# Kernel optimization log

Hardware: AMD Instinct MI355X
Metric: run time of the kernel (lower is better)

## Reference

```python
import jax, jax.numpy as jnp
import numpy as np

SEQ_LEN = 4096
PRED_LEN = 4096
D_MODEL = 512
PERIOD = 32
N = SEQ_LEN // PERIOD   # 128
M = PRED_LEN // PERIOD  # 128
K = 2 * (PERIOD // 2) + 1  # 33
B = 32


def setup_inputs() -> dict:
    key = jax.random.key(0)
    k1, k2, k3 = jax.random.split(key, 3)
    h = jax.random.normal(k1, (B, SEQ_LEN, D_MODEL), dtype=jnp.float32)
    # torch Conv1d weight layout: [out_ch, in_ch/groups, k] = [D, 1, K]
    conv_w = jax.random.normal(k2, (D_MODEL, 1, K), dtype=jnp.float32) * (1.0 / np.sqrt(K))
    # torch Linear(n, m, bias=False) weight: [m, n]
    backbone_w = jax.random.normal(k3, (M, N), dtype=jnp.float32) * (1.0 / np.sqrt(N))
    return {"h": h, "conv_w": conv_w, "backbone_w": backbone_w}


def reference(h, conv_w, backbone_w):
    Bb, L, D = h.shape
    w, n, m, H = PERIOD, N, M, PRED_LEN
    h_t = jnp.transpose(h, (0, 2, 1))  # [B, D, L]
    conv = jax.lax.conv_general_dilated(
        h_t, conv_w,
        window_strides=(1,),
        padding=[(K // 2, K // 2)],
        dimension_numbers=("NCH", "OIH", "NCH"),
        feature_group_count=D,
    )
    h_agg = h_t + conv  # residual depthwise conv, [B, D, L]
    # rearrange into phases: [B*D, n, w] -> [B*D, w, n]
    x_by_phase = jnp.transpose(h_agg.reshape(Bb * D, n, w), (0, 2, 1))
    # per-phase linear n -> m (Linear weight is [m, n], applied as x @ W^T)
    y_by_phase = jnp.einsum("pwn,mn->pwm", x_by_phase, backbone_w)  # [B*D, w, m]
    # de-interleave phases back into a length-H sequence
    y_reordered = jnp.transpose(y_by_phase, (0, 2, 1)).reshape(Bb * D, H)
    y = jnp.transpose(y_reordered.reshape(Bb, D, H), (0, 2, 1))  # [B, H, D]
    return y
```

## Files before the change

### kernel.cpp

```cpp
#include <hip/hip_runtime.h>

#define SEQ_LEN 4096
#define D_MODEL 512
#define KSZ 33

typedef __attribute__((ext_vector_type(4))) float float4v;
typedef __attribute__((ext_vector_type(8))) short short8;

static __device__ __forceinline__ unsigned short f2bf(float f) {
    unsigned int u = __float_as_uint(f);
    u += 0x7fffu + ((u >> 16) & 1u);
    return (unsigned short)(u >> 16);
}

__global__ __launch_bounds__(256) void k_prep(const float* __restrict__ bw,
                                              unsigned short* __restrict__ wb) {
    int i = blockIdx.x * 256 + threadIdx.x;
    if (i < 128 * 128) wb[i] = f2bf(bw[i]);
}

__global__ __launch_bounds__(256) void k_conv(const float* __restrict__ h,
                                              const float* __restrict__ cw,
                                              float* __restrict__ hagg) {
    __shared__ float tile[96][64];
    __shared__ float wsh[64][33];

    const int lt = blockIdx.x, dt = blockIdx.y, b = blockIdx.z;
    const int tid = threadIdx.x;
    const int c = tid & 63;
    const int l0 = lt * 64;

    const float* hb = h + ((size_t)b * SEQ_LEN) * D_MODEL + dt * 64;
    for (int r = (tid >> 6); r < 96; r += 4) {
        int l = l0 - 16 + r;
        float v = 0.f;
        if (l >= 0 && l < SEQ_LEN) v = hb[(size_t)l * D_MODEL + c];
        tile[r][c] = v;
    }
    for (int idx = tid; idx < 64 * KSZ; idx += 256) {
        int dd = idx / KSZ, k = idx - dd * KSZ;
        wsh[dd][k] = cw[(size_t)(dt * 64 + dd) * KSZ + k];
    }
    __syncthreads();

    const int lsub = (tid >> 6) * 16;

    float buf[16];
#pragma unroll
    for (int j = 0; j < 16; j++) buf[j] = tile[lsub + j][c];

    float acc[16] = {};
#pragma unroll
    for (int k = 0; k < KSZ; k++) {
        float wk = wsh[c][k] + ((k == 16) ? 1.0f : 0.0f);
#pragma unroll
        for (int j = 0; j < 16; j++) acc[j] += wk * buf[(k + j) & 15];
        if (k < 32) buf[k & 15] = tile[lsub + k + 16][c];
    }

    float* ob = hagg + ((size_t)b * SEQ_LEN + l0 + lsub) * D_MODEL + dt * 64 + c;
#pragma unroll
    for (int j = 0; j < 16; j++) ob[(size_t)j * D_MODEL] = acc[j];
}

#define XSTR 136
__global__ __launch_bounds__(256, 2) void k_gemm(const unsigned short* __restrict__ wb,
                                                 float* __restrict__ outp) {
    __shared__ unsigned short xl[256 * XSTR];

    const int tid = threadIdx.x;
    const int dh = blockIdx.x, ph = blockIdx.y, b = blockIdx.z;
    const int lane = tid & 63, w = tid >> 6;

    {
        const float* xrow0 = outp + ((size_t)(b * SEQ_LEN) + ph) * D_MODEL
                           + dh * 256 + lane * 4;
#pragma unroll
        for (int p = 0; p < 16; p++) {
            int ip = p * 4 + w;
            int i0 = ip * 2;
            const float* src = xrow0 + (size_t)i0 * 32 * D_MODEL;
            float4v v0 = *(const float4v*)(src);
            float4v v1 = *(const float4v*)(src + 32 * D_MODEL);
            int ib = i0 >> 3;
            int wof = i0 & 7;
#pragma unroll
            for (int dd = 0; dd < 4; dd++) {
                int d = lane * 4 + dd;
                unsigned int pk = (unsigned int)f2bf(v0[dd])
                                | ((unsigned int)f2bf(v1[dd]) << 16);
                int off = d * XSTR + (((ib ^ (d >> 3)) & 15) << 3) + wof;
                *(unsigned int*)(&xl[off]) = pk;
            }
        }
    }
    __syncthreads();

    const int q = lane >> 4, r16 = lane & 15;

    float4v acc[2][16] = {};
#pragma unroll
    for (int kb = 0; kb < 128; kb += 32) {
        short8 a[2];
#pragma unroll
        for (int mt = 0; mt < 2; mt++) {
            int row = w * 32 + mt * 16 + r16;
            a[mt] = *(const short8*)(wb + row * 128 + kb + q * 8);
        }
#pragma unroll
        for (int dtl = 0; dtl < 16; dtl++) {
            int d = dtl * 16 + r16;
            int ib = (kb >> 3) + q;
            short8 bfrag = *(const short8*)(&xl[d * XSTR + (((ib ^ (d >> 3)) & 15) << 3)]);
#pragma unroll
            for (int mt = 0; mt < 2; mt++)
                acc[mt][dtl] = __builtin_amdgcn_mfma_f32_16x16x32_bf16(
                    a[mt], bfrag, acc[mt][dtl], 0, 0, 0);
        }
    }

    float* ob = outp + ((size_t)b * SEQ_LEN) * D_MODEL;
#pragma unroll
    for (int mt = 0; mt < 2; mt++) {
        int mbase = w * 32 + mt * 16 + q * 4;
#pragma unroll
        for (int r = 0; r < 4; r++) {
            int m = mbase + r;
            int hidx = m * 32 + ph;
#pragma unroll
            for (int dtl = 0; dtl < 16; dtl++) {
                int d = dh * 256 + dtl * 16 + r16;
                ob[(size_t)hidx * D_MODEL + d] = acc[mt][dtl][r];
            }
        }
    }
}

extern "C" void kernel_launch(void* const* d_in, const int* in_sizes, int n_in,
                              void* d_out, int out_size, void* d_ws, size_t ws_size,
                              hipStream_t stream) {
    const float* h  = (const float*)d_in[0];
    const float* cw = (const float*)d_in[1];
    const float* bw = (const float*)d_in[2];
    float* out = (float*)d_out;

    unsigned short* wb = (unsigned short*)d_ws;

    k_prep<<<dim3(64), 256, 0, stream>>>(bw, wb);
    k_conv<<<dim3(64, 8, 32), 256, 0, stream>>>(h, cw, out);
    k_gemm<<<dim3(2, 32, 32), 256, 0, stream>>>(wb, out);
}
```

Baseline: 740.9 us.

## Transpose conv weights in prep, widen GEMM blocks, and stage output stores through LDS

The prep kernel now writes a transposed copy of the conv weights, so the conv kernel reads per-channel weights directly with coalesced global loads instead of staging them in shared memory. Empty asm barriers keep the input buffer values pinned in registers. The GEMM kernel moves to 512 threads with one 16-row M tile per wave, batches its global loads before the bf16 conversion, and writes its output through an LDS transpose so each wave issues float4 row stores instead of scattered scalar stores. This adds extra barriers and LDS traffic in exchange for better-coalesced output writes and higher occupancy.

Measured after the change: 693.7 us. 6.4% less time.

```diff
diff --git a/kernel.cpp b/kernel.cpp
--- a/kernel.cpp
+++ b/kernel.cpp
@@ -14,16 +14,21 @@
 }
 
 __global__ __launch_bounds__(256) void k_prep(const float* __restrict__ bw,
-                                              unsigned short* __restrict__ wb) {
+                                              const float* __restrict__ cw,
+                                              unsigned short* __restrict__ wb,
+                                              float* __restrict__ wt) {
     int i = blockIdx.x * 256 + threadIdx.x;
     if (i < 128 * 128) wb[i] = f2bf(bw[i]);
+    if (i < KSZ * D_MODEL) {
+        int k = i >> 9, d = i & 511;
+        wt[i] = cw[(size_t)d * KSZ + k];
+    }
 }
 
 __global__ __launch_bounds__(256) void k_conv(const float* __restrict__ h,
-                                              const float* __restrict__ cw,
+                                              const float* __restrict__ wt,
                                               float* __restrict__ hagg) {
     __shared__ float tile[96][64];
-    __shared__ float wsh[64][33];
 
     const int lt = blockIdx.x, dt = blockIdx.y, b = blockIdx.z;
     const int tid = threadIdx.x;
@@ -37,25 +42,28 @@
         if (l >= 0 && l < SEQ_LEN) v = hb[(size_t)l * D_MODEL + c];
         tile[r][c] = v;
     }
-    for (int idx = tid; idx < 64 * KSZ; idx += 256) {
-        int dd = idx / KSZ, k = idx - dd * KSZ;
-        wsh[dd][k] = cw[(size_t)(dt * 64 + dd) * KSZ + k];
-    }
     __syncthreads();
 
     const int lsub = (tid >> 6) * 16;
+    const float* wcol = wt + dt * 64 + c;
 
     float buf[16];
 #pragma unroll
-    for (int j = 0; j < 16; j++) buf[j] = tile[lsub + j][c];
+    for (int j = 0; j < 16; j++) {
+        buf[j] = tile[lsub + j][c];
+        asm volatile("" : "+v"(buf[j]));
+    }
 
     float acc[16] = {};
 #pragma unroll
     for (int k = 0; k < KSZ; k++) {
-        float wk = wsh[c][k] + ((k == 16) ? 1.0f : 0.0f);
+        float wk = wcol[(size_t)k * D_MODEL] + ((k == 16) ? 1.0f : 0.0f);
 #pragma unroll
         for (int j = 0; j < 16; j++) acc[j] += wk * buf[(k + j) & 15];
-        if (k < 32) buf[k & 15] = tile[lsub + k + 16][c];
+        if (k < 32) {
+            buf[k & 15] = tile[lsub + k + 16][c];
+            asm volatile("" : "+v"(buf[k & 15]));
+        }
     }
 
     float* ob = hagg + ((size_t)b * SEQ_LEN + l0 + lsub) * D_MODEL + dt * 64 + c;
@@ -64,9 +72,9 @@
 }
 
 #define XSTR 136
-__global__ __launch_bounds__(256, 2) void k_gemm(const unsigned short* __restrict__ wb,
+__global__ __launch_bounds__(512, 4) void k_gemm(const unsigned short* __restrict__ wb,
                                                  float* __restrict__ outp) {
-    __shared__ unsigned short xl[256 * XSTR];
+    __shared__ __attribute__((aligned(16))) unsigned short xl[256 * XSTR];
 
     const int tid = threadIdx.x;
     const int dh = blockIdx.x, ph = blockIdx.y, b = blockIdx.z;
@@ -76,21 +84,27 @@
         const float* xrow0 = outp + ((size_t)(b * SEQ_LEN) + ph) * D_MODEL
                            + dh * 256 + lane * 4;
 #pragma unroll
-        for (int p = 0; p < 16; p++) {
-            int ip = p * 4 + w;
-            int i0 = ip * 2;
-            const float* src = xrow0 + (size_t)i0 * 32 * D_MODEL;
-            float4v v0 = *(const float4v*)(src);
-            float4v v1 = *(const float4v*)(src + 32 * D_MODEL);
-            int ib = i0 >> 3;
-            int wof = i0 & 7;
+        for (int c2 = 0; c2 < 2; c2++) {
+            float4v va[4], vb[4];
 #pragma unroll
-            for (int dd = 0; dd < 4; dd++) {
-                int d = lane * 4 + dd;
-                unsigned int pk = (unsigned int)f2bf(v0[dd])
-                                | ((unsigned int)f2bf(v1[dd]) << 16);
-                int off = d * XSTR + (((ib ^ (d >> 3)) & 15) << 3) + wof;
-                *(unsigned int*)(&xl[off]) = pk;
+            for (int pp = 0; pp < 4; pp++) {
+                int ip = (c2 * 4 + pp) * 8 + w;
+                const float* src = xrow0 + (size_t)(ip * 2) * 32 * D_MODEL;
+                va[pp] = *(const float4v*)(src);
+                vb[pp] = *(const float4v*)(src + 32 * D_MODEL);
+            }
+#pragma unroll
+            for (int pp = 0; pp < 4; pp++) {
+                int i0 = ((c2 * 4 + pp) * 8 + w) * 2;
+                int ib = i0 >> 3, wof = i0 & 7;
+#pragma unroll
+                for (int dd = 0; dd < 4; dd++) {
+                    int d = lane * 4 + dd;
+                    unsigned int pk = (unsigned int)f2bf(va[pp][dd])
+                                    | ((unsigned int)f2bf(vb[pp][dd]) << 16);
+                    int off = d * XSTR + (((ib ^ (d >> 3)) & 15) << 3) + wof;
+                    *(unsigned int*)(&xl[off]) = pk;
+                }
             }
         }
     }
@@ -98,41 +112,41 @@
 
     const int q = lane >> 4, r16 = lane & 15;
 
-    float4v acc[2][16] = {};
+    float4v acc[16] = {};
 #pragma unroll
     for (int kb = 0; kb < 128; kb += 32) {
-        short8 a[2];
-#pragma unroll
-        for (int mt = 0; mt < 2; mt++) {
-            int row = w * 32 + mt * 16 + r16;
-            a[mt] = *(const short8*)(wb + row * 128 + kb + q * 8);
-        }
+        short8 a = *(const short8*)(wb + (w * 16 + r16) * 128 + kb + q * 8);
 #pragma unroll
         for (int dtl = 0; dtl < 16; dtl++) {
             int d = dtl * 16 + r16;
             int ib = (kb >> 3) + q;
             short8 bfrag = *(const short8*)(&xl[d * XSTR + (((ib ^ (d >> 3)) & 15) << 3)]);
-#pragma unroll
-            for (int mt = 0; mt < 2; mt++)
-                acc[mt][dtl] = __builtin_amdgcn_mfma_f32_16x16x32_bf16(
-                    a[mt], bfrag, acc[mt][dtl], 0, 0, 0);
+            acc[dtl] = __builtin_amdgcn_mfma_f32_16x16x32_bf16(a, bfrag, acc[dtl], 0, 0, 0);
         }
     }
+    __syncthreads();
 
+    float* yt = (float*)xl;
     float* ob = outp + ((size_t)b * SEQ_LEN) * D_MODEL;
 #pragma unroll
-    for (int mt = 0; mt < 2; mt++) {
-        int mbase = w * 32 + mt * 16 + q * 4;
+    for (int half = 0; half < 2; half++) {
+        if ((w >> 2) == half) {
+            int mloc = (w & 3) * 16 + q * 4;
 #pragma unroll
-        for (int r = 0; r < 4; r++) {
-            int m = mbase + r;
-            int hidx = m * 32 + ph;
+            for (int dtl = 0; dtl < 16; dtl++)
 #pragma unroll
-            for (int dtl = 0; dtl < 16; dtl++) {
-                int d = dh * 256 + dtl * 16 + r16;
-                ob[(size_t)hidx * D_MODEL + d] = acc[mt][dtl][r];
-            }
+                for (int r = 0; r < 4; r++)
+                    yt[(mloc + r) * 260 + dtl * 16 + r16] = acc[dtl][r];
         }
+        __syncthreads();
+#pragma unroll
+        for (int it = 0; it < 8; it++) {
+            int row = it * 8 + w;
+            float4v v = *(const float4v*)(&yt[row * 260 + lane * 4]);
+            int m = half * 64 + row;
+            *(float4v*)(ob + ((size_t)(m * 32 + ph)) * D_MODEL + dh * 256 + lane * 4) = v;
+        }
+        __syncthreads();
     }
 }
 
@@ -145,8 +159,9 @@
     float* out = (float*)d_out;
 
     unsigned short* wb = (unsigned short*)d_ws;
+    float* wt = (float*)((char*)d_ws + 32768);
 
-    k_prep<<<dim3(64), 256, 0, stream>>>(bw, wb);
-    k_conv<<<dim3(64, 8, 32), 256, 0, stream>>>(h, cw, out);
-    k_gemm<<<dim3(2, 32, 32), 256, 0, stream>>>(wb, out);
+    k_prep<<<dim3(66), 256, 0, stream>>>(bw, cw, wb, wt);
+    k_conv<<<dim3(64, 8, 32), 256, 0, stream>>>(h, wt, out);
+    k_gemm<<<dim3(2, 32, 32), 512, 0, stream>>>(wb, out);
 }
```
